# Performance work log

Hardware: AMD Instinct MI355X
Metric: run time of the kernel (lower is better)

The kernel has to match this reference:

```python
import jax, jax.numpy as jnp
import numpy as np

HEAD_SIZE = 128
BLOCK_SIZE = 2048


def setup_inputs() -> dict:
    key = jax.random.key(0)
    kx, kk, kq, kv = jax.random.split(key, 4)
    B, T, C = 8, 2048, HEAD_SIZE
    s = 1.0 / np.sqrt(C)
    x = jax.random.normal(kx, (B, T, C), dtype=jnp.float32)
    Wk = jax.random.normal(kk, (C, C), dtype=jnp.float32) * s
    Wq = jax.random.normal(kq, (C, C), dtype=jnp.float32) * s
    Wv = jax.random.normal(kv, (C, C), dtype=jnp.float32) * s
    return {"x": x, "Wk": Wk, "Wq": Wq, "Wv": Wv}


def reference(x, Wk, Wq, Wv):
    B, T, C = x.shape
    # nn.Linear(C, C, bias=False): y = x @ W.T
    k = jnp.einsum('btc,dc->btd', x, Wk)
    q = jnp.einsum('btc,dc->btd', x, Wq)
    v = jnp.einsum('btc,dc->btd', x, Wv)
    scores = jnp.einsum('btd,bsd->bts', q, k) * (C ** -0.5)  # [B,T,T]
    causal = jnp.tril(jnp.ones((T, T), dtype=bool))
    scores = jnp.where(causal, scores, -jnp.inf)
    weights = jax.nn.softmax(scores, axis=-1)
    return jnp.einsum('bts,bsd->btd', weights, v)
```

## Files before the change

kernel.cpp:

```cpp
#include <hip/hip_runtime.h>

#define T_SEQ 2048
#define C_DIM 128
#define S_QK 0.08838834764831845f

typedef __attribute__((ext_vector_type(8))) short bf16x8;
typedef __attribute__((ext_vector_type(4))) float f32x4;

#define OPART_OFF 12582912UL
#define ML_OFF    31457280UL

#define GLOAD_LDS16(gp, lp)                                          \
    __builtin_amdgcn_global_load_lds(                                \
        (const __attribute__((address_space(1))) void*)(gp),         \
        (__attribute__((address_space(3))) void*)(lp), 16, 0, 0)

__device__ __forceinline__ unsigned short f2bf(float f) {
    union { float f; unsigned int u; } v; v.f = f;
    unsigned int r = v.u + 0x7FFFu + ((v.u >> 16) & 1u);
    return (unsigned short)(r >> 16);
}

__device__ __forceinline__ int chunk_base(int qt) {
    int g = qt >> 3;
    if (g == 1) return (qt - 8) * 2;
    if (g == 2) return 16 + (qt - 16) * 3;
    return 40 + (qt - 24) * 4;
}

__global__ __launch_bounds__(256) void proj_kernel(
    const float* __restrict__ x,
    const float* __restrict__ Wk, const float* __restrict__ Wq,
    const float* __restrict__ Wv,
    unsigned short* __restrict__ qo, unsigned short* __restrict__ ko,
    unsigned short* __restrict__ vto)
{
    const int rt = blockIdx.x;
    const int z  = blockIdx.y;
    const int tid  = threadIdx.x;
    const int lane = tid & 63;
    const int w    = tid >> 6;
    const int n16  = lane & 15;
    const int quad = lane >> 4;

    __shared__ __align__(16) unsigned short Wl[128 * 136];
    __shared__ __align__(16) unsigned short Xl[9216];

    const float* Wsrc = (z == 0 ? Wq : z == 1 ? Wk : Wv);
    const float wscale = (z == 0) ? S_QK : 1.0f;
    #pragma unroll
    for (int i = 0; i < 16; ++i) {
        int e = (tid + i * 256) * 4;
        int r = e >> 7, c = e & 127;
        float4 v = *reinterpret_cast<const float4*>(Wsrc + e);
        ushort4 o4;
        o4.x = f2bf(v.x * wscale); o4.y = f2bf(v.y * wscale);
        o4.z = f2bf(v.z * wscale); o4.w = f2bf(v.w * wscale);
        *reinterpret_cast<ushort4*>(&Wl[r * 136 + c]) = o4;
    }
    const float* xrow = x + (size_t)rt * 64 * C_DIM;
    #pragma unroll
    for (int i = 0; i < 8; ++i) {
        int e = (tid + i * 256) * 4;
        int r = e >> 7, c = e & 127;
        float4 v = *reinterpret_cast<const float4*>(xrow + e);
        ushort4 o4;
        o4.x = f2bf(v.x); o4.y = f2bf(v.y);
        o4.z = f2bf(v.z); o4.w = f2bf(v.w);
        *reinterpret_cast<ushort4*>(&Xl[r * 136 + c]) = o4;
    }
    __syncthreads();

    const int arow = w * 16 + n16;
    bf16x8 afr[4];
    #pragma unroll
    for (int kk = 0; kk < 4; ++kk)
        afr[kk] = *reinterpret_cast<const bf16x8*>(&Xl[arow * 136 + kk * 32 + quad * 8]);

    f32x4 acc[8];
    #pragma unroll
    for (int nt = 0; nt < 8; ++nt) acc[nt] = (f32x4){0.f, 0.f, 0.f, 0.f};
    #pragma unroll
    for (int kk = 0; kk < 4; ++kk)
        #pragma unroll
        for (int nt = 0; nt < 8; ++nt) {
            bf16x8 bfr = *reinterpret_cast<const bf16x8*>(
                &Wl[(nt * 16 + n16) * 136 + kk * 32 + quad * 8]);
            acc[nt] = __builtin_amdgcn_mfma_f32_16x16x32_bf16(afr[kk], bfr, acc[nt], 0, 0, 0);
        }

    const int trow_base = w * 16 + quad * 4;
    __syncthreads();
    if (z < 2) {
        #pragma unroll
        for (int nt = 0; nt < 8; ++nt)
            #pragma unroll
            for (int r = 0; r < 4; ++r)
                Xl[(trow_base + r) * 136 + nt * 16 + n16] = f2bf(acc[nt][r]);
        __syncthreads();
        unsigned short* dst = (z == 0 ? qo : ko) + (size_t)rt * 64 * C_DIM;
        #pragma unroll
        for (int i = 0; i < 4; ++i) {
            int e = (tid + i * 256) * 8;
            int r = e >> 7, c = e & 127;
            *reinterpret_cast<uint4*>(dst + e) =
                *reinterpret_cast<const uint4*>(&Xl[r * 136 + c]);
        }
    } else {
        const int b  = rt >> 5;
        const int qt = rt & 31;
        #pragma unroll
        for (int nt = 0; nt < 8; ++nt)
            #pragma unroll
            for (int r = 0; r < 4; ++r)
                Xl[(nt * 16 + n16) * 72 + trow_base + r] = f2bf(acc[nt][r]);
        __syncthreads();
        unsigned short* dst = vto + (size_t)b * C_DIM * T_SEQ + (size_t)qt * 64;
        #pragma unroll
        for (int i = 0; i < 4; ++i) {
            int e = tid + i * 256;
            int d = e >> 3, cv = (e & 7) * 8;
            *reinterpret_cast<uint4*>(dst + (size_t)d * T_SEQ + cv) =
                *reinterpret_cast<const uint4*>(&Xl[d * 72 + cv]);
        }
    }
}

__device__ __forceinline__ void stage_tile32(
    const char* ksb, const char* vsb,
    unsigned short* klbuf, unsigned short* vlbuf, int tid, int w)
{
    #pragma unroll
    for (int it = 0; it < 2; ++it) {
        const int L = it * 256 + tid;
        const int r = L >> 4, c = L & 15;
        GLOAD_LDS16(ksb + r * 256 + ((c ^ (r & 7)) << 4),
                    klbuf + (size_t)(it * 256 + w * 64) * 8);
    }
    #pragma unroll
    for (int it = 0; it < 2; ++it) {
        const int L = it * 256 + tid;
        const int r = L >> 2, c = L & 3;
        GLOAD_LDS16(vsb + (size_t)r * (T_SEQ * 2) +
                        ((c ^ (r & 3) ^ ((r >> 2) & 3)) << 4),
                    vlbuf + (size_t)(it * 256 + w * 64) * 8);
    }
}

__global__ __launch_bounds__(256, 4) void attn_kernel(
    const unsigned short* __restrict__ qb,
    const unsigned short* __restrict__ kb,
    const unsigned short* __restrict__ vtb,
    float* __restrict__ opart, float2* __restrict__ mlbuf,
    float* __restrict__ out)
{
    const int lin   = blockIdx.x;
    const int b     = lin & 7;
    const int rest  = lin >> 3;
    const int qt    = rest & 31;
    const int chunk = rest >> 5;
    if (chunk * 8 > qt) return;

    const int tid  = threadIdx.x;
    const int lane = tid & 63;
    const int w    = tid >> 6;
    const int n16  = lane & 15;
    const int quad = lane >> 4;

    __shared__ __align__(16) unsigned short Kl[2][32 * 128];
    __shared__ __align__(16) unsigned short Vl[2][128 * 32];
    __shared__ __align__(16) unsigned short Pl[4][16 * 40];

    const size_t bT = (size_t)b * T_SEQ;
    const int qbase = qt * 64 + w * 16;
    const int qabs  = qbase + n16;

    const int st0 = chunk * 16;
    const int st1 = min(chunk * 16 + 16, 2 * qt + 2);

    const char* kbase = (const char*)(kb + bT * C_DIM);
    const char* vbase = (const char*)(vtb + (size_t)b * C_DIM * T_SEQ);

    stage_tile32(kbase + (size_t)st0 * 8192, vbase + (size_t)st0 * 64,
                 Kl[0], Vl[0], tid, w);

    bf16x8 qfr[4];
    #pragma unroll
    for (int kk = 0; kk < 4; ++kk)
        qfr[kk] = *reinterpret_cast<const bf16x8*>(
            qb + (bT + qbase + n16) * C_DIM + kk * 32 + quad * 8);

    f32x4 o[8];
    #pragma unroll
    for (int ct = 0; ct < 8; ++ct) o[ct] = (f32x4){0.f, 0.f, 0.f, 0.f};
    float m_ = -INFINITY, l_ = 0.f;

    unsigned short* pw = Pl[w];
    const int vswz = (quad ^ (n16 & 3) ^ ((n16 >> 2) & 3)) * 8;

    int cur = 0;
    for (int st = st0; st < st1; ++st, cur ^= 1) {
        if (st + 1 < st1) {
            stage_tile32(kbase + (size_t)(st + 1) * 8192,
                         vbase + (size_t)(st + 1) * 64,
                         Kl[cur ^ 1], Vl[cur ^ 1], tid, w);
            asm volatile("s_waitcnt vmcnt(4)" ::: "memory");
        } else {
            asm volatile("s_waitcnt vmcnt(0)" ::: "memory");
        }
        __builtin_amdgcn_s_barrier();

        const unsigned short* klc = Kl[cur];
        const unsigned short* vlc = Vl[cur];

        f32x4 s[2];
        s[0] = (f32x4){0.f, 0.f, 0.f, 0.f};
        s[1] = (f32x4){0.f, 0.f, 0.f, 0.f};
        #pragma unroll
        for (int kk = 0; kk < 4; ++kk)
            #pragma unroll
            for (int nt = 0; nt < 2; ++nt) {
                bf16x8 kfr = *reinterpret_cast<const bf16x8*>(
                    &klc[(nt * 16 + n16) * 128 + (((kk * 4 + quad) ^ (n16 & 7)) * 8)]);
                s[nt] = __builtin_amdgcn_mfma_f32_16x16x32_bf16(kfr, qfr[kk], s[nt], 0, 0, 0);
            }

        if (st >= 2 * qt) {
            #pragma unroll
            for (int nt = 0; nt < 2; ++nt)
                #pragma unroll
                for (int r = 0; r < 4; ++r) {
                    int sabs = st * 32 + nt * 16 + quad * 4 + r;
                    if (sabs > qabs) s[nt][r] = -1e30f;
                }
        }

        float pmax = fmaxf(fmaxf(fmaxf(s[0][0], s[0][1]), fmaxf(s[0][2], s[0][3])),
                           fmaxf(fmaxf(s[1][0], s[1][1]), fmaxf(s[1][2], s[1][3])));
        pmax = fmaxf(pmax, __shfl_xor(pmax, 16));
        pmax = fmaxf(pmax, __shfl_xor(pmax, 32));
        float mn = fmaxf(m_, pmax);
        float alpha = __expf(m_ - mn);
        float tsum = 0.f;
        #pragma unroll
        for (int nt = 0; nt < 2; ++nt)
            #pragma unroll
            for (int r = 0; r < 4; ++r) {
                float p = __expf(s[nt][r] - mn);
                s[nt][r] = p;
                tsum += p;
            }
        tsum += __shfl_xor(tsum, 16);
        tsum += __shfl_xor(tsum, 32);
        l_ = l_ * alpha + tsum;
        m_ = mn;
        #pragma unroll
        for (int ct = 0; ct < 8; ++ct) {
            o[ct][0] *= alpha; o[ct][1] *= alpha;
            o[ct][2] *= alpha; o[ct][3] *= alpha;
        }

        #pragma unroll
        for (int nt = 0; nt < 2; ++nt) {
            ushort4 pk;
            pk.x = f2bf(s[nt][0]); pk.y = f2bf(s[nt][1]);
            pk.z = f2bf(s[nt][2]); pk.w = f2bf(s[nt][3]);
            *reinterpret_cast<ushort4*>(&pw[n16 * 40 + nt * 16 + quad * 4]) = pk;
        }

        bf16x8 pfr = *reinterpret_cast<const bf16x8*>(&pw[n16 * 40 + quad * 8]);
        #pragma unroll
        for (int ct = 0; ct < 8; ++ct) {
            bf16x8 vfr = *reinterpret_cast<const bf16x8*>(
                &vlc[(ct * 16 + n16) * 32 + vswz]);
            o[ct] = __builtin_amdgcn_mfma_f32_16x16x32_bf16(vfr, pfr, o[ct], 0, 0, 0);
        }

        asm volatile("s_waitcnt lgkmcnt(0)" ::: "memory");
        __builtin_amdgcn_s_barrier();
    }

    if (qt < 8) {
        float* outp = out + (bT + qbase + n16) * C_DIM;
        const float inv = 1.0f / l_;
        #pragma unroll
        for (int ct = 0; ct < 8; ++ct) {
            float4 r4;
            r4.x = o[ct][0] * inv; r4.y = o[ct][1] * inv;
            r4.z = o[ct][2] * inv; r4.w = o[ct][3] * inv;
            *reinterpret_cast<float4*>(outp + ct * 16 + quad * 4) = r4;
        }
    } else {
        const int slot = b * 72 + chunk_base(qt) + chunk;
        float* op = opart + (size_t)slot * 8192 + (size_t)(w * 16 + n16) * 128;
        #pragma unroll
        for (int ct = 0; ct < 8; ++ct) {
            float4 r4;
            r4.x = o[ct][0]; r4.y = o[ct][1];
            r4.z = o[ct][2]; r4.w = o[ct][3];
            *reinterpret_cast<float4*>(op + ct * 16 + quad * 4) = r4;
        }
        if (quad == 0)
            mlbuf[(size_t)slot * 64 + w * 16 + n16] = make_float2(m_, l_);
    }
}

__global__ __launch_bounds__(256) void merge_kernel(
    const float* __restrict__ opart, const float2* __restrict__ mlbuf,
    float* __restrict__ out)
{
    const int qt = 8 + blockIdx.x;
    const int b  = blockIdx.y;
    const int nch  = (qt >> 3) + 1;
    const int base = b * 72 + chunk_base(qt);
    const int row = threadIdx.x >> 2;
    const int c0  = (threadIdx.x & 3) * 32;

    float mi[4], li[4], wgt[4];
    float M = -INFINITY;
    for (int i = 0; i < nch; ++i) {
        float2 t = mlbuf[(size_t)(base + i) * 64 + row];
        mi[i] = t.x; li[i] = t.y;
        M = fmaxf(M, t.x);
    }
    float L = 0.f;
    for (int i = 0; i < nch; ++i) {
        wgt[i] = __expf(mi[i] - M);
        L += li[i] * wgt[i];
    }
    const float inv = 1.0f / L;

    float* orow = out + ((size_t)(b * T_SEQ + qt * 64 + row)) * C_DIM;
    #pragma unroll
    for (int j = 0; j < 8; ++j) {
        int col = c0 + j * 4;
        float ax = 0.f, ay = 0.f, az = 0.f, aw = 0.f;
        for (int i = 0; i < nch; ++i) {
            float4 p = *reinterpret_cast<const float4*>(
                opart + (size_t)(base + i) * 8192 + row * 128 + col);
            ax += wgt[i] * p.x; ay += wgt[i] * p.y;
            az += wgt[i] * p.z; aw += wgt[i] * p.w;
        }
        float4 r4; r4.x = ax * inv; r4.y = ay * inv; r4.z = az * inv; r4.w = aw * inv;
        *reinterpret_cast<float4*>(orow + col) = r4;
    }
}

extern "C" void kernel_launch(void* const* d_in, const int* in_sizes, int n_in,
                              void* d_out, int out_size, void* d_ws, size_t ws_size,
                              hipStream_t stream) {
    const float* x  = (const float*)d_in[0];
    const float* Wk = (const float*)d_in[1];
    const float* Wq = (const float*)d_in[2];
    const float* Wv = (const float*)d_in[3];

    unsigned short* qw  = (unsigned short*)d_ws;
    unsigned short* kw  = qw + 2097152;
    unsigned short* vw  = kw + 2097152;
    float*          opart = (float*)((char*)d_ws + OPART_OFF);
    float2*         mlb   = (float2*)((char*)d_ws + ML_OFF);

    proj_kernel<<<dim3(256, 3), 256, 0, stream>>>(x, Wk, Wq, Wv, qw, kw, vw);
    attn_kernel<<<dim3(1024), 256, 0, stream>>>(qw, kw, vw, opart, mlb, (float*)d_out);
    merge_kernel<<<dim3(24, 8), 256, 0, stream>>>(opart, mlb, (float*)d_out);
}
```

Baseline: 122.6 us.

## Fuse merge into attention via atomic counters and keep P in registers

Removes the separate merge kernel: the last chunk block for each query tile, detected with an atomic counter reset in the projection kernel, combines the partial outputs itself. The attention inner loop now works on 16-key sub-tiles and passes P through registers into 16x16x16 bf16 MFMAs instead of going through LDS. It also skips fully masked sub-tiles per wave, rescales the running max only when it rises by more than 8, raises wave priority around the MFMAs, and uses hardware packed bf16 conversion. The lazy rescale lets exponentials grow up to e^8 before renormalising, and the fused merge adds fences and atomics.

```diff
diff --git a/kernel.cpp b/kernel.cpp
--- a/kernel.cpp
+++ b/kernel.cpp
@@ -5,10 +5,12 @@
 #define S_QK 0.08838834764831845f
 
 typedef __attribute__((ext_vector_type(8))) short bf16x8;
+typedef __attribute__((ext_vector_type(4))) short bf16x4;
 typedef __attribute__((ext_vector_type(4))) float f32x4;
 
 #define OPART_OFF 12582912UL
 #define ML_OFF    31457280UL
+#define CNT_OFF   31752192UL
 
 #define GLOAD_LDS16(gp, lp)                                          \
     __builtin_amdgcn_global_load_lds(                                \
@@ -19,6 +21,19 @@
     union { float f; unsigned int u; } v; v.f = f;
     unsigned int r = v.u + 0x7FFFu + ((v.u >> 16) & 1u);
     return (unsigned short)(r >> 16);
+}
+
+__device__ __forceinline__ f32x4 mfma16(bf16x4 a, bf16x4 b, f32x4 c) {
+#if __has_builtin(__builtin_amdgcn_mfma_f32_16x16x16_bf16_1k)
+    return __builtin_amdgcn_mfma_f32_16x16x16_bf16_1k(a, b, c, 0, 0, 0);
+#elif __has_builtin(__builtin_amdgcn_mfma_f32_16x16x16_bf16)
+    return __builtin_amdgcn_mfma_f32_16x16x16_bf16(a, b, c, 0, 0, 0);
+#else
+    f32x4 d = c;
+    asm volatile("v_mfma_f32_16x16x16_bf16 %0, %1, %2, %0"
+                 : "+v"(d) : "v"(a), "v"(b));
+    return d;
+#endif
 }
 
 __device__ __forceinline__ int chunk_base(int qt) {
@@ -33,7 +48,7 @@
     const float* __restrict__ Wk, const float* __restrict__ Wq,
     const float* __restrict__ Wv,
     unsigned short* __restrict__ qo, unsigned short* __restrict__ ko,
-    unsigned short* __restrict__ vto)
+    unsigned short* __restrict__ vto, unsigned* __restrict__ cnt)
 {
     const int rt = blockIdx.x;
     const int z  = blockIdx.y;
@@ -43,6 +58,8 @@
     const int n16  = lane & 15;
     const int quad = lane >> 4;
 
+    if (rt == 0 && z == 0) cnt[tid] = 0;
+
     __shared__ __align__(16) unsigned short Wl[128 * 136];
     __shared__ __align__(16) unsigned short Xl[9216];
 
@@ -53,10 +70,13 @@
         int e = (tid + i * 256) * 4;
         int r = e >> 7, c = e & 127;
         float4 v = *reinterpret_cast<const float4*>(Wsrc + e);
-        ushort4 o4;
-        o4.x = f2bf(v.x * wscale); o4.y = f2bf(v.y * wscale);
-        o4.z = f2bf(v.z * wscale); o4.w = f2bf(v.w * wscale);
-        *reinterpret_cast<ushort4*>(&Wl[r * 136 + c]) = o4;
+        float ax = v.x * wscale, ay = v.y * wscale;
+        float az = v.z * wscale, aw = v.w * wscale;
+        unsigned lo, hi;
+        asm("v_cvt_pk_bf16_f32 %0, %1, %2" : "=v"(lo) : "v"(ax), "v"(ay));
+        asm("v_cvt_pk_bf16_f32 %0, %1, %2" : "=v"(hi) : "v"(az), "v"(aw));
+        uint2 o2; o2.x = lo; o2.y = hi;
+        *reinterpret_cast<uint2*>(&Wl[r * 136 + c]) = o2;
     }
     const float* xrow = x + (size_t)rt * 64 * C_DIM;
     #pragma unroll
@@ -64,10 +84,11 @@
         int e = (tid + i * 256) * 4;
         int r = e >> 7, c = e & 127;
         float4 v = *reinterpret_cast<const float4*>(xrow + e);
-        ushort4 o4;
-        o4.x = f2bf(v.x); o4.y = f2bf(v.y);
-        o4.z = f2bf(v.z); o4.w = f2bf(v.w);
-        *reinterpret_cast<ushort4*>(&Xl[r * 136 + c]) = o4;
+        unsigned lo, hi;
+        asm("v_cvt_pk_bf16_f32 %0, %1, %2" : "=v"(lo) : "v"(v.x), "v"(v.y));
+        asm("v_cvt_pk_bf16_f32 %0, %1, %2" : "=v"(hi) : "v"(v.z), "v"(v.w));
+        uint2 o2; o2.x = lo; o2.y = hi;
+        *reinterpret_cast<uint2*>(&Xl[r * 136 + c]) = o2;
     }
     __syncthreads();
 
@@ -152,6 +173,7 @@
     const unsigned short* __restrict__ kb,
     const unsigned short* __restrict__ vtb,
     float* __restrict__ opart, float2* __restrict__ mlbuf,
+    unsigned* __restrict__ cnt,
     float* __restrict__ out)
 {
     const int lin   = blockIdx.x;
@@ -169,11 +191,11 @@
 
     __shared__ __align__(16) unsigned short Kl[2][32 * 128];
     __shared__ __align__(16) unsigned short Vl[2][128 * 32];
-    __shared__ __align__(16) unsigned short Pl[4][16 * 40];
+    __shared__ int lastflag;
 
     const size_t bT = (size_t)b * T_SEQ;
     const int qbase = qt * 64 + w * 16;
-    const int qabs  = qbase + n16;
+    const int ulim  = 4 * qt + w;
 
     const int st0 = chunk * 16;
     const int st1 = min(chunk * 16 + 16, 2 * qt + 2);
@@ -195,8 +217,10 @@
     for (int ct = 0; ct < 8; ++ct) o[ct] = (f32x4){0.f, 0.f, 0.f, 0.f};
     float m_ = -INFINITY, l_ = 0.f;
 
-    unsigned short* pw = Pl[w];
-    const int vswz = (quad ^ (n16 & 3) ^ ((n16 >> 2) & 3)) * 8;
+    const int kx  = n16 & 7;
+    const int sig = (n16 & 3) ^ ((n16 >> 2) & 3);
+    const int vof0 = n16 * 32 + (((quad >> 1) ^ sig) << 3) + (quad & 1) * 4;
+    const int vof1 = n16 * 32 + ((((quad >> 1) + 2) ^ sig) << 3) + (quad & 1) * 4;
 
     int cur = 0;
     for (int st = st0; st < st1; ++st, cur ^= 1) {
@@ -213,67 +237,64 @@
         const unsigned short* klc = Kl[cur];
         const unsigned short* vlc = Vl[cur];
 
-        f32x4 s[2];
-        s[0] = (f32x4){0.f, 0.f, 0.f, 0.f};
-        s[1] = (f32x4){0.f, 0.f, 0.f, 0.f};
-        #pragma unroll
-        for (int kk = 0; kk < 4; ++kk)
-            #pragma unroll
-            for (int nt = 0; nt < 2; ++nt) {
-                bf16x8 kfr = *reinterpret_cast<const bf16x8*>(
-                    &klc[(nt * 16 + n16) * 128 + (((kk * 4 + quad) ^ (n16 & 7)) * 8)]);
-                s[nt] = __builtin_amdgcn_mfma_f32_16x16x32_bf16(kfr, qfr[kk], s[nt], 0, 0, 0);
+        #pragma unroll
+        for (int sub = 0; sub < 2; ++sub) {
+            const int u = st * 2 + sub;
+            if (u <= ulim) {
+                f32x4 s4 = (f32x4){0.f, 0.f, 0.f, 0.f};
+                const unsigned short* krow = klc + (sub * 16 + n16) * 128;
+                __builtin_amdgcn_s_setprio(1);
+                #pragma unroll
+                for (int kk = 0; kk < 4; ++kk) {
+                    bf16x8 kfr = *reinterpret_cast<const bf16x8*>(
+                        krow + (((kk * 4 + quad) ^ kx) << 3));
+                    s4 = __builtin_amdgcn_mfma_f32_16x16x32_bf16(kfr, qfr[kk], s4, 0, 0, 0);
+                }
+                __builtin_amdgcn_s_setprio(0);
+
+                if (u == ulim) {
+                    #pragma unroll
+                    for (int r = 0; r < 4; ++r) {
+                        int sabs = u * 16 + quad * 4 + r;
+                        if (sabs > qbase + n16) s4[r] = -1e30f;
+                    }
+                }
+
+                float pmax = fmaxf(fmaxf(s4[0], s4[1]), fmaxf(s4[2], s4[3]));
+                pmax = fmaxf(pmax, __shfl_xor(pmax, 16));
+                pmax = fmaxf(pmax, __shfl_xor(pmax, 32));
+                if (pmax > m_ + 8.f) {
+                    float alpha = __expf(m_ - pmax);
+                    l_ *= alpha;
+                    #pragma unroll
+                    for (int ct = 0; ct < 8; ++ct) {
+                        o[ct][0] *= alpha; o[ct][1] *= alpha;
+                        o[ct][2] *= alpha; o[ct][3] *= alpha;
+                    }
+                    m_ = pmax;
+                }
+                float p0 = __expf(s4[0] - m_), p1 = __expf(s4[1] - m_);
+                float p2 = __expf(s4[2] - m_), p3 = __expf(s4[3] - m_);
+                float ts = (p0 + p1) + (p2 + p3);
+                ts += __shfl_xor(ts, 16);
+                ts += __shfl_xor(ts, 32);
+                l_ += ts;
+
+                unsigned plo, phi;
+                asm("v_cvt_pk_bf16_f32 %0, %1, %2" : "=v"(plo) : "v"(p0), "v"(p1));
+                asm("v_cvt_pk_bf16_f32 %0, %1, %2" : "=v"(phi) : "v"(p2), "v"(p3));
+                union { unsigned u2[2]; bf16x4 v; } pu;
+                pu.u2[0] = plo; pu.u2[1] = phi;
+
+                const int vof = sub ? vof1 : vof0;
+                __builtin_amdgcn_s_setprio(1);
+                #pragma unroll
+                for (int ct = 0; ct < 8; ++ct) {
+                    bf16x4 vfr = *reinterpret_cast<const bf16x4*>(vlc + ct * 512 + vof);
+                    o[ct] = mfma16(vfr, pu.v, o[ct]);
+                }
+                __builtin_amdgcn_s_setprio(0);
             }
-
-        if (st >= 2 * qt) {
-            #pragma unroll
-            for (int nt = 0; nt < 2; ++nt)
-                #pragma unroll
-                for (int r = 0; r < 4; ++r) {
-                    int sabs = st * 32 + nt * 16 + quad * 4 + r;
-                    if (sabs > qabs) s[nt][r] = -1e30f;
-                }
-        }
-
-        float pmax = fmaxf(fmaxf(fmaxf(s[0][0], s[0][1]), fmaxf(s[0][2], s[0][3])),
-                           fmaxf(fmaxf(s[1][0], s[1][1]), fmaxf(s[1][2], s[1][3])));
-        pmax = fmaxf(pmax, __shfl_xor(pmax, 16));
-        pmax = fmaxf(pmax, __shfl_xor(pmax, 32));
-        float mn = fmaxf(m_, pmax);
-        float alpha = __expf(m_ - mn);
-        float tsum = 0.f;
-        #pragma unroll
-        for (int nt = 0; nt < 2; ++nt)
-            #pragma unroll
-            for (int r = 0; r < 4; ++r) {
-                float p = __expf(s[nt][r] - mn);
-                s[nt][r] = p;
-                tsum += p;
-            }
-        tsum += __shfl_xor(tsum, 16);
-        tsum += __shfl_xor(tsum, 32);
-        l_ = l_ * alpha + tsum;
-        m_ = mn;
-        #pragma unroll
-        for (int ct = 0; ct < 8; ++ct) {
-            o[ct][0] *= alpha; o[ct][1] *= alpha;
-            o[ct][2] *= alpha; o[ct][3] *= alpha;
-        }
-
-        #pragma unroll
-        for (int nt = 0; nt < 2; ++nt) {
-            ushort4 pk;
-            pk.x = f2bf(s[nt][0]); pk.y = f2bf(s[nt][1]);
-            pk.z = f2bf(s[nt][2]); pk.w = f2bf(s[nt][3]);
-            *reinterpret_cast<ushort4*>(&pw[n16 * 40 + nt * 16 + quad * 4]) = pk;
-        }
-
-        bf16x8 pfr = *reinterpret_cast<const bf16x8*>(&pw[n16 * 40 + quad * 8]);
-        #pragma unroll
-        for (int ct = 0; ct < 8; ++ct) {
-            bf16x8 vfr = *reinterpret_cast<const bf16x8*>(
-                &vlc[(ct * 16 + n16) * 32 + vswz]);
-            o[ct] = __builtin_amdgcn_mfma_f32_16x16x32_bf16(vfr, pfr, o[ct], 0, 0, 0);
         }
 
         asm volatile("s_waitcnt lgkmcnt(0)" ::: "memory");
@@ -290,58 +311,66 @@
             r4.z = o[ct][2] * inv; r4.w = o[ct][3] * inv;
             *reinterpret_cast<float4*>(outp + ct * 16 + quad * 4) = r4;
         }
-    } else {
-        const int slot = b * 72 + chunk_base(qt) + chunk;
-        float* op = opart + (size_t)slot * 8192 + (size_t)(w * 16 + n16) * 128;
-        #pragma unroll
-        for (int ct = 0; ct < 8; ++ct) {
-            float4 r4;
-            r4.x = o[ct][0]; r4.y = o[ct][1];
-            r4.z = o[ct][2]; r4.w = o[ct][3];
-            *reinterpret_cast<float4*>(op + ct * 16 + quad * 4) = r4;
-        }
-        if (quad == 0)
-            mlbuf[(size_t)slot * 64 + w * 16 + n16] = make_float2(m_, l_);
-    }
-}
-
-__global__ __launch_bounds__(256) void merge_kernel(
-    const float* __restrict__ opart, const float2* __restrict__ mlbuf,
-    float* __restrict__ out)
-{
-    const int qt = 8 + blockIdx.x;
-    const int b  = blockIdx.y;
+        return;
+    }
+
     const int nch  = (qt >> 3) + 1;
     const int base = b * 72 + chunk_base(qt);
-    const int row = threadIdx.x >> 2;
-    const int c0  = (threadIdx.x & 3) * 32;
-
-    float mi[4], li[4], wgt[4];
-    float M = -INFINITY;
-    for (int i = 0; i < nch; ++i) {
-        float2 t = mlbuf[(size_t)(base + i) * 64 + row];
-        mi[i] = t.x; li[i] = t.y;
-        M = fmaxf(M, t.x);
-    }
-    float L = 0.f;
-    for (int i = 0; i < nch; ++i) {
-        wgt[i] = __expf(mi[i] - M);
-        L += li[i] * wgt[i];
-    }
+    const int slot = base + chunk;
+    float* op = opart + (size_t)slot * 8192 + (size_t)(w * 16 + n16) * 128;
+    #pragma unroll
+    for (int ct = 0; ct < 8; ++ct) {
+        float4 r4;
+        r4.x = o[ct][0]; r4.y = o[ct][1];
+        r4.z = o[ct][2]; r4.w = o[ct][3];
+        *reinterpret_cast<float4*>(op + ct * 16 + quad * 4) = r4;
+    }
+    if (quad == 0)
+        mlbuf[(size_t)slot * 64 + w * 16 + n16] = make_float2(m_, l_);
+
+    __threadfence();
+    __syncthreads();
+    if (tid == 0) {
+        unsigned old = atomicAdd(&cnt[b * 32 + qt], 1u);
+        lastflag = (old == (unsigned)(nch - 1));
+    }
+    __syncthreads();
+    if (!lastflag) return;
+    __threadfence();
+
+    const int row = tid >> 2;
+    const int c0  = (tid & 3) * 32;
+    float2 t0 = mlbuf[(size_t)(base + 0) * 64 + row];
+    float2 t1 = mlbuf[(size_t)(base + 1) * 64 + row];
+    float2 t2 = (nch > 2) ? mlbuf[(size_t)(base + 2) * 64 + row]
+                          : make_float2(-INFINITY, 0.f);
+    float2 t3 = (nch > 3) ? mlbuf[(size_t)(base + 3) * 64 + row]
+                          : make_float2(-INFINITY, 0.f);
+    float M = fmaxf(fmaxf(t0.x, t1.x), fmaxf(t2.x, t3.x));
+    float w0 = __expf(t0.x - M), w1 = __expf(t1.x - M);
+    float w2 = __expf(t2.x - M), w3 = __expf(t3.x - M);
+    float L = t0.y * w0 + t1.y * w1 + t2.y * w2 + t3.y * w3;
     const float inv = 1.0f / L;
 
     float* orow = out + ((size_t)(b * T_SEQ + qt * 64 + row)) * C_DIM;
     #pragma unroll
     for (int j = 0; j < 8; ++j) {
         int col = c0 + j * 4;
-        float ax = 0.f, ay = 0.f, az = 0.f, aw = 0.f;
-        for (int i = 0; i < nch; ++i) {
-            float4 p = *reinterpret_cast<const float4*>(
-                opart + (size_t)(base + i) * 8192 + row * 128 + col);
-            ax += wgt[i] * p.x; ay += wgt[i] * p.y;
-            az += wgt[i] * p.z; aw += wgt[i] * p.w;
-        }
-        float4 r4; r4.x = ax * inv; r4.y = ay * inv; r4.z = az * inv; r4.w = aw * inv;
+        const float* p0p = opart + (size_t)(base + 0) * 8192 + row * 128 + col;
+        const float* p1p = opart + (size_t)(base + 1) * 8192 + row * 128 + col;
+        float4 a0 = *reinterpret_cast<const float4*>(p0p);
+        float4 a1 = *reinterpret_cast<const float4*>(p1p);
+        float4 a2 = (nch > 2) ? *reinterpret_cast<const float4*>(
+                        opart + (size_t)(base + 2) * 8192 + row * 128 + col)
+                              : make_float4(0.f, 0.f, 0.f, 0.f);
+        float4 a3 = (nch > 3) ? *reinterpret_cast<const float4*>(
+                        opart + (size_t)(base + 3) * 8192 + row * 128 + col)
+                              : make_float4(0.f, 0.f, 0.f, 0.f);
+        float4 r4;
+        r4.x = (a0.x * w0 + a1.x * w1 + a2.x * w2 + a3.x * w3) * inv;
+        r4.y = (a0.y * w0 + a1.y * w1 + a2.y * w2 + a3.y * w3) * inv;
+        r4.z = (a0.z * w0 + a1.z * w1 + a2.z * w2 + a3.z * w3) * inv;
+        r4.w = (a0.w * w0 + a1.w * w1 + a2.w * w2 + a3.w * w3) * inv;
         *reinterpret_cast<float4*>(orow + col) = r4;
     }
 }
@@ -359,8 +388,8 @@
     unsigned short* vw  = kw + 2097152;
     float*          opart = (float*)((char*)d_ws + OPART_OFF);
     float2*         mlb   = (float2*)((char*)d_ws + ML_OFF);
-
-    proj_kernel<<<dim3(256, 3), 256, 0, stream>>>(x, Wk, Wq, Wv, qw, kw, vw);
-    attn_kernel<<<dim3(1024), 256, 0, stream>>>(qw, kw, vw, opart, mlb, (float*)d_out);
-    merge_kernel<<<dim3(24, 8), 256, 0, stream>>>(opart, mlb, (float*)d_out);
-}
+    unsigned*       cnt   = (unsigned*)((char*)d_ws + CNT_OFF);
+
+    proj_kernel<<<dim3(256, 3), 256, 0, stream>>>(x, Wk, Wq, Wv, qw, kw, vw, cnt);
+    attn_kernel<<<dim3(1024), 256, 0, stream>>>(qw, kw, vw, opart, mlb, cnt, (float*)d_out);
+}
```

Result: slower. 212.2 us (+73.0%).
